# Kernel tuning notes

Hardware: AMD Instinct MI355X
Metric: run time of the kernel (lower is better)

Reference implementation:

```python
import jax, jax.numpy as jnp
import numpy as np

D_MODEL, D_FF, RANK = 1024, 4096, 256
B, S = 4, 4096


def setup_inputs() -> dict:
    key = jax.random.key(0)
    ks = jax.random.split(key, 7)
    return {
        "x":  jax.random.normal(ks[0], (B, S, D_MODEL), dtype=jnp.float32),
        "U1": jax.random.normal(ks[1], (D_MODEL, RANK), dtype=jnp.float32) * 0.02,
        "V1": jax.random.normal(ks[2], (RANK, D_FF), dtype=jnp.float32) * 0.02,
        "b1": jnp.zeros((D_FF,), dtype=jnp.float32),
        "U2": jax.random.normal(ks[3], (D_FF, RANK), dtype=jnp.float32) * 0.02,
        "V2": jax.random.normal(ks[4], (RANK, D_MODEL), dtype=jnp.float32) * 0.02,
        "b2": jnp.zeros((D_MODEL,), dtype=jnp.float32),
    }


def reference(x, U1, V1, b1, U2, V2, b2):
    # P = x @ U1  -> low-rank projection [B, S, rank]
    P = jnp.einsum("bsd,dr->bsr", x, U1)
    # H = gelu(P @ V1 + b1)  -> [B, S, d_ff] (the intermediate the flash kernel tiles over)
    H = jax.nn.gelu(jnp.einsum("bsr,rf->bsf", P, V1) + b1)
    # Q = H @ U2 -> [B, S, rank]; out = Q @ V2 + b2 -> [B, S, d_model]
    Q = jnp.einsum("bsf,fr->bsr", H, U2)
    return jnp.einsum("bsr,rd->bsd", Q, V2) + b2
```

## Files before the change

### kernel.cpp

```cpp
#include <hip/hip_runtime.h>
#include <hip/hip_bf16.h>


typedef __attribute__((ext_vector_type(8))) short bfrag8;
typedef __attribute__((ext_vector_type(4))) float fx4;
typedef __attribute__((ext_vector_type(4))) unsigned short usx4;

#define D_MODEL 1024
#define D_FF    4096
#define RANK    256
#define NROWS   16384
#define PSTR    264
#define XSTR    136

__device__ __forceinline__ unsigned short f2b(float f) {
  union { float f; unsigned u; } v; v.f = f;
  unsigned r = v.u + 0x7FFFu + ((v.u >> 16) & 1u);
  return (unsigned short)(r >> 16);
}

__device__ __forceinline__ float gelu_tanh(float x) {
  float x2 = x * x;
  float inner = __builtin_fmaf(0.044715f * x2, x, x);
  float e = __expf(1.5957691216057308f * inner);
  float t = __builtin_fmaf(-2.0f, __builtin_amdgcn_rcpf(1.0f + e), 1.0f);
  float hx = 0.5f * x;
  return __builtin_fmaf(hx, t, hx);
}

__device__ __forceinline__ void gl_lds16(const unsigned short* g, unsigned short* l) {
  __builtin_amdgcn_global_load_lds(
      (const __attribute__((address_space(1))) unsigned int*)g,
      (__attribute__((address_space(3))) unsigned int*)l, 16, 0, 0);
}

__global__ void tconv(const float* __restrict__ in, unsigned short* __restrict__ out,
                      int R, int C) {
  __shared__ float t[32][33];
  int c0 = blockIdx.x * 32, r0 = blockIdx.y * 32;
  int tx = threadIdx.x & 31, ty = threadIdx.x >> 5;
#pragma unroll
  for (int i = 0; i < 32; i += 8)
    t[ty + i][tx] = in[(size_t)(r0 + ty + i) * C + c0 + tx];
  __syncthreads();
#pragma unroll
  for (int i = 0; i < 32; i += 8)
    out[(size_t)(c0 + ty + i) * R + r0 + tx] = f2b(t[tx][ty + i]);
}

__global__ void v1pack(const float* __restrict__ in, unsigned short* __restrict__ out) {
  __shared__ float t[32][33];
  int f0 = blockIdx.x * 32, k0 = blockIdx.y * 32;
  int tx = threadIdx.x & 31, ty = threadIdx.x >> 5;
#pragma unroll
  for (int i = 0; i < 32; i += 8)
    t[ty + i][tx] = in[(size_t)(k0 + ty + i) * D_FF + f0 + tx];
  __syncthreads();
#pragma unroll
  for (int i = 0; i < 32; i += 8) {
    int f = ty + i;
    out[(size_t)(f0 + f) * RANK + ((k0 + tx) ^ ((f & 7) << 3))] = f2b(t[tx][f]);
  }
}

__global__ void u2pack(const float* __restrict__ in, unsigned short* __restrict__ out) {
  __shared__ float t[32][33];
  int f0 = blockIdx.x * 32, r0 = blockIdx.y * 32;
  int cg = blockIdx.x;
  int tx = threadIdx.x & 31, ty = threadIdx.x >> 5;
#pragma unroll
  for (int i = 0; i < 32; i += 8)
    t[ty + i][tx] = in[(size_t)(f0 + ty + i) * RANK + r0 + tx];
  __syncthreads();
#pragma unroll
  for (int i = 0; i < 32; i += 8) {
    int r2l = ty + i;
    int s = tx ^ (((r2l >> 1) & 3) << 3);
    int fl = (((s & 7) >= 4) ? 16 : 0) + 4 * (s >> 3) + (s & 3);
    out[(size_t)cg * 8192 + (size_t)(r0 + r2l) * 32 + tx] = f2b(t[fl][r2l]);
  }
}

__global__ __launch_bounds__(256, 4) void pgemm(
    const float* __restrict__ x, const unsigned short* __restrict__ u1t,
    unsigned short* __restrict__ P)
{
  __shared__ unsigned short xs[32 * XSTR];
  const int tid = threadIdx.x;
  const int w = tid >> 6, lane = tid & 63, lo = lane & 15, hi = lane >> 4;
  const size_t gr0 = (size_t)blockIdx.x * 32;

  fx4 acc[2][4];
#pragma unroll
  for (int mt = 0; mt < 2; ++mt)
#pragma unroll
    for (int nt = 0; nt < 4; ++nt) acc[mt][nt] = fx4{0.f, 0.f, 0.f, 0.f};

  for (int d0 = 0; d0 < D_MODEL; d0 += 128) {
    __syncthreads();
#pragma unroll
    for (int it = 0; it < 4; ++it) {
      int idx = it * 256 + tid;
      int r = idx >> 5, c = (idx & 31) << 2;
      fx4 v = *(const fx4*)(x + (gr0 + r) * D_MODEL + d0 + c);
      usx4 bv; bv[0] = f2b(v[0]); bv[1] = f2b(v[1]); bv[2] = f2b(v[2]); bv[3] = f2b(v[3]);
      *(usx4*)(xs + r * XSTR + c) = bv;
    }
    __syncthreads();
#pragma unroll
    for (int ks = 0; ks < 128; ks += 32) {
      bfrag8 a[2], b[4];
#pragma unroll
      for (int mt = 0; mt < 2; ++mt)
        a[mt] = *(const bfrag8*)(xs + (16 * mt + lo) * XSTR + ks + hi * 8);
#pragma unroll
      for (int nt = 0; nt < 4; ++nt)
        b[nt] = *(const bfrag8*)(u1t + (size_t)(w * 64 + nt * 16 + lo) * D_MODEL + d0 + ks + hi * 8);
#pragma unroll
      for (int mt = 0; mt < 2; ++mt)
#pragma unroll
        for (int nt = 0; nt < 4; ++nt)
          acc[mt][nt] = __builtin_amdgcn_mfma_f32_16x16x32_bf16(a[mt], b[nt], acc[mt][nt], 0, 0, 0);
    }
  }
#pragma unroll
  for (int mt = 0; mt < 2; ++mt)
#pragma unroll
    for (int nt = 0; nt < 4; ++nt)
#pragma unroll
      for (int r = 0; r < 4; ++r)
        P[(gr0 + 16 * mt + 4 * hi + r) * RANK + w * 64 + nt * 16 + lo] = f2b(acc[mt][nt][r]);
}

__global__ __launch_bounds__(256, 2) void hqgemm(
    const unsigned short* __restrict__ P,
    const unsigned short* __restrict__ v1c,
    const float* __restrict__ b1,
    const unsigned short* __restrict__ u2c,
    float* __restrict__ qpart,
    int F)
{
  __shared__ unsigned short v1s[2][32 * 256];
  __shared__ unsigned short u2s[2][256 * 32];

  const int tid = threadIdx.x;
  const int w = tid >> 6, lane = tid & 63, lo = lane & 15, hi = lane >> 4;

  int bid = blockIdx.x, j = 0, rb = bid;
  if (F == 4)      { j = bid & 3; rb = bid >> 2; }
  else if (F == 2) { j = bid & 1; rb = bid >> 1; }
  const int fbase = j * (D_FF / F);
  const int nchunk = (D_FF / F) / 32;
  const int rowstart = rb * 128 + w * 32;

  bfrag8 pf[2][8];
#pragma unroll
  for (int rg = 0; rg < 2; ++rg)
#pragma unroll
    for (int ks = 0; ks < 8; ++ks)
      pf[rg][ks] = *(const bfrag8*)(P + (size_t)(rowstart + 16 * rg + lo) * RANK + ks * 32 + hi * 8);

  fx4 qacc[2][16];
#pragma unroll
  for (int rg = 0; rg < 2; ++rg)
#pragma unroll
    for (int nt = 0; nt < 16; ++nt) qacc[rg][nt] = fx4{0.f, 0.f, 0.f, 0.f};

  const int vswz = (lo & 7) << 3;
  const int qoff = (hi * 8) ^ (((lo >> 1) & 3) << 3);
  const int vbase = lo * 256;

  {
    const unsigned short* vsrc = v1c + (size_t)fbase * 256;
    const unsigned short* usrc = u2c + (size_t)(fbase >> 5) * 8192;
#pragma unroll
    for (int p = 0; p < 4; ++p) {
      int off = tid * 8 + p * 2048;
      gl_lds16(vsrc + off, &v1s[0][off]);
      gl_lds16(usrc + off, &u2s[0][off]);
    }
  }
  __syncthreads();

  int cur = 0;
  for (int c = 0; c < nchunk; ++c) {
    if (c + 1 < nchunk) {
      const unsigned short* vsrc = v1c + (size_t)(fbase + (c + 1) * 32) * 256;
      const unsigned short* usrc = u2c + (size_t)((fbase >> 5) + c + 1) * 8192;
#pragma unroll
      for (int p = 0; p < 4; ++p) {
        int off = tid * 8 + p * 2048;
        gl_lds16(vsrc + off, &v1s[cur ^ 1][off]);
        gl_lds16(usrc + off, &u2s[cur ^ 1][off]);
      }
    }
    const unsigned short* vb = v1s[cur];
    const unsigned short* ub = u2s[cur];

    fx4 hacc[2][2];
#pragma unroll
    for (int t = 0; t < 2; ++t)
#pragma unroll
      for (int rg = 0; rg < 2; ++rg) hacc[t][rg] = fx4{0.f, 0.f, 0.f, 0.f};
#pragma unroll
    for (int ks = 0; ks < 8; ++ks) {
      int ko = (ks * 32 + hi * 8) ^ vswz;
      bfrag8 vE = *(const bfrag8*)(vb + vbase + ko);
      bfrag8 vO = *(const bfrag8*)(vb + vbase + 4096 + ko);
      hacc[0][0] = __builtin_amdgcn_mfma_f32_16x16x32_bf16(vE, pf[0][ks], hacc[0][0], 0, 0, 0);
      hacc[0][1] = __builtin_amdgcn_mfma_f32_16x16x32_bf16(vE, pf[1][ks], hacc[0][1], 0, 0, 0);
      hacc[1][0] = __builtin_amdgcn_mfma_f32_16x16x32_bf16(vO, pf[0][ks], hacc[1][0], 0, 0, 0);
      hacc[1][1] = __builtin_amdgcn_mfma_f32_16x16x32_bf16(vO, pf[1][ks], hacc[1][1], 0, 0, 0);
    }

    const int f0g = fbase + c * 32;
    fx4 bE = *(const fx4*)(b1 + f0g + 4 * hi);
    fx4 bO = *(const fx4*)(b1 + f0g + 16 + 4 * hi);
    bfrag8 bq0, bq1;
#pragma unroll
    for (int r = 0; r < 4; ++r) {
      bq0[r]     = (short)f2b(gelu_tanh(hacc[0][0][r] + bE[r]));
      bq0[r + 4] = (short)f2b(gelu_tanh(hacc[1][0][r] + bO[r]));
      bq1[r]     = (short)f2b(gelu_tanh(hacc[0][1][r] + bE[r]));
      bq1[r + 4] = (short)f2b(gelu_tanh(hacc[1][1][r] + bO[r]));
    }

#pragma unroll
    for (int nt = 0; nt < 16; ++nt) {
      bfrag8 qa = *(const bfrag8*)(ub + (16 * nt + lo) * 32 + qoff);
      qacc[0][nt] = __builtin_amdgcn_mfma_f32_16x16x32_bf16(qa, bq0, qacc[0][nt], 0, 0, 0);
      qacc[1][nt] = __builtin_amdgcn_mfma_f32_16x16x32_bf16(qa, bq1, qacc[1][nt], 0, 0, 0);
    }

    __syncthreads();
    cur ^= 1;
  }

  float* qp = qpart + (size_t)j * NROWS * RANK;
#pragma unroll
  for (int rg = 0; rg < 2; ++rg) {
    size_t row = (size_t)(rowstart + 16 * rg + lo);
#pragma unroll
    for (int nt = 0; nt < 16; ++nt)
      *(fx4*)(qp + row * RANK + 16 * nt + 4 * hi) = qacc[rg][nt];
  }
}

__global__ __launch_bounds__(512, 4) void ogemm(
    const float* __restrict__ qpart, int F,
    const unsigned short* __restrict__ v2t,
    const float* __restrict__ b2,
    float* __restrict__ out)
{
  __shared__ unsigned short Qs[64 * PSTR];
  const int tid = threadIdx.x;
  const int w = tid >> 6, lane = tid & 63, lo = lane & 15, hi = lane >> 4;
  const int wm = w >> 2, wn = w & 3;
  const size_t gr0 = (size_t)blockIdx.x * 64;
  const int n0 = blockIdx.y * 256;

#pragma unroll
  for (int it = 0; it < 8; ++it) {
    int idx = it * 512 + tid;
    int r = idx >> 6, c = (idx & 63) << 2;
    fx4 s = *(const fx4*)(qpart + (gr0 + r) * RANK + c);
    for (int jj = 1; jj < F; ++jj) {
      fx4 s1 = *(const fx4*)(qpart + (size_t)jj * NROWS * RANK + (gr0 + r) * RANK + c);
      s[0] += s1[0]; s[1] += s1[1]; s[2] += s1[2]; s[3] += s1[3];
    }
    usx4 bv; bv[0] = f2b(s[0]); bv[1] = f2b(s[1]); bv[2] = f2b(s[2]); bv[3] = f2b(s[3]);
    *(usx4*)(Qs + r * PSTR + c) = bv;
  }
  __syncthreads();

  fx4 acc[2][4];
#pragma unroll
  for (int mt = 0; mt < 2; ++mt)
#pragma unroll
    for (int nt = 0; nt < 4; ++nt) acc[mt][nt] = fx4{0.f, 0.f, 0.f, 0.f};

#pragma unroll
  for (int ks = 0; ks < RANK; ks += 32) {
    bfrag8 a[2], b[4];
#pragma unroll
    for (int mt = 0; mt < 2; ++mt)
      a[mt] = *(const bfrag8*)(Qs + (wm * 32 + 16 * mt + lo) * PSTR + ks + hi * 8);
#pragma unroll
    for (int nt = 0; nt < 4; ++nt)
      b[nt] = *(const bfrag8*)(v2t + (size_t)(n0 + wn * 64 + nt * 16 + lo) * RANK + ks + hi * 8);
#pragma unroll
    for (int mt = 0; mt < 2; ++mt)
#pragma unroll
      for (int nt = 0; nt < 4; ++nt)
        acc[mt][nt] = __builtin_amdgcn_mfma_f32_16x16x32_bf16(a[mt], b[nt], acc[mt][nt], 0, 0, 0);
  }

#pragma unroll
  for (int nt = 0; nt < 4; ++nt) {
    int col = n0 + wn * 64 + nt * 16 + lo;
    float bias = b2[col];
#pragma unroll
    for (int mt = 0; mt < 2; ++mt)
#pragma unroll
      for (int r = 0; r < 4; ++r)
        out[(gr0 + wm * 32 + 16 * mt + 4 * hi + r) * D_MODEL + col] = acc[mt][nt][r] + bias;
  }
}

extern "C" void kernel_launch(void* const* d_in, const int* in_sizes, int n_in,
                              void* d_out, int out_size, void* d_ws, size_t ws_size,
                              hipStream_t stream) {
  const float* x  = (const float*)d_in[0];
  const float* U1 = (const float*)d_in[1];
  const float* V1 = (const float*)d_in[2];
  const float* b1 = (const float*)d_in[3];
  const float* U2 = (const float*)d_in[4];
  const float* V2 = (const float*)d_in[5];
  const float* b2 = (const float*)d_in[6];
  float* out = (float*)d_out;

  unsigned short* ws16 = (unsigned short*)d_ws;
  unsigned short* u1t = ws16;
  unsigned short* v1c = u1t + (size_t)RANK * D_MODEL;
  unsigned short* u2c = v1c + (size_t)D_FF * RANK;
  unsigned short* v2t = u2c + (size_t)RANK * D_FF;
  unsigned short* Pbf = v2t + (size_t)D_MODEL * RANK;
  float* qpart = (float*)(Pbf + (size_t)NROWS * RANK);

  size_t fixed_bytes = 2ull * ((size_t)RANK * D_MODEL + (size_t)D_FF * RANK +
                               (size_t)RANK * D_FF + (size_t)D_MODEL * RANK +
                               (size_t)NROWS * RANK);
  size_t qbytes = (size_t)NROWS * RANK * 4;
  int F = 1;
  if      (ws_size >= fixed_bytes + 4 * qbytes) F = 4;
  else if (ws_size >= fixed_bytes + 2 * qbytes) F = 2;

  tconv<<<dim3(RANK / 32, D_MODEL / 32), 256, 0, stream>>>(U1, u1t, D_MODEL, RANK);
  v1pack<<<dim3(D_FF / 32, RANK / 32), 256, 0, stream>>>(V1, v1c);
  u2pack<<<dim3(D_FF / 32, RANK / 32), 256, 0, stream>>>(U2, u2c);
  tconv<<<dim3(D_MODEL / 32, RANK / 32), 256, 0, stream>>>(V2, v2t, RANK, D_MODEL);

  pgemm<<<NROWS / 32, 256, 0, stream>>>(x, u1t, Pbf);
  hqgemm<<<(NROWS / 128) * F, 256, 0, stream>>>(Pbf, v1c, b1, u2c, qpart, F);
  ogemm<<<dim3(NROWS / 64, D_MODEL / 256), 512, 0, stream>>>(qpart, F, v2t, b2, out);
}
```

Measured before the change: 202.5 us.

## Deepen hqgemm prefetch pipeline, store bf16 partials, and split F up to eight

Rewrites the hqgemm loop to keep two chunks in flight, using explicit vmcnt waits and raw barriers in place of __syncthreads, and adds s_setprio around the MFMA blocks. The bias is staged in LDS and GELU now uses exp2. Partial Q sums are stored as bf16 instead of fp32, which halves partial-sum traffic and lets F rise to 8 for more blocks in flight. The trade-off is extra rounding error in the partial sums and a fallback to F=4 that assumes enough workspace without checking.

Result: slower. 216.9 us (+7.1%).

```diff
diff --git a/kernel.cpp b/kernel.cpp
--- a/kernel.cpp
+++ b/kernel.cpp
@@ -18,11 +18,14 @@
   unsigned r = v.u + 0x7FFFu + ((v.u >> 16) & 1u);
   return (unsigned short)(r >> 16);
 }
+__device__ __forceinline__ float b2f(unsigned short u) {
+  union { unsigned u; float f; } v; v.u = ((unsigned)u) << 16; return v.f;
+}
 
 __device__ __forceinline__ float gelu_tanh(float x) {
   float x2 = x * x;
   float inner = __builtin_fmaf(0.044715f * x2, x, x);
-  float e = __expf(1.5957691216057308f * inner);
+  float e = __builtin_amdgcn_exp2f(2.302118885f * inner);
   float t = __builtin_fmaf(-2.0f, __builtin_amdgcn_rcpf(1.0f + e), 1.0f);
   float hx = 0.5f * x;
   return __builtin_fmaf(hx, t, hx);
@@ -137,20 +140,22 @@
     const unsigned short* __restrict__ v1c,
     const float* __restrict__ b1,
     const unsigned short* __restrict__ u2c,
-    float* __restrict__ qpart,
+    unsigned short* __restrict__ qpart,
     int F)
 {
   __shared__ unsigned short v1s[2][32 * 256];
   __shared__ unsigned short u2s[2][256 * 32];
+  __shared__ float b1s[1024];
 
   const int tid = threadIdx.x;
   const int w = tid >> 6, lane = tid & 63, lo = lane & 15, hi = lane >> 4;
 
-  int bid = blockIdx.x, j = 0, rb = bid;
-  if (F == 4)      { j = bid & 3; rb = bid >> 2; }
-  else if (F == 2) { j = bid & 1; rb = bid >> 1; }
-  const int fbase = j * (D_FF / F);
-  const int nchunk = (D_FF / F) / 32;
+  const int bid = blockIdx.x;
+  const int j = bid % F;
+  const int rb = bid / F;
+  const int fspan = D_FF / F;
+  const int fbase = j * fspan;
+  const int nchunk = fspan / 32;
   const int rowstart = rb * 128 + w * 32;
 
   bfrag8 pf[2][8];
@@ -159,6 +164,8 @@
 #pragma unroll
     for (int ks = 0; ks < 8; ++ks)
       pf[rg][ks] = *(const bfrag8*)(P + (size_t)(rowstart + 16 * rg + lo) * RANK + ks * 32 + hi * 8);
+  for (int i = tid; i < fspan; i += 256) b1s[i] = b1[fbase + i];
+  __syncthreads();
 
   fx4 qacc[2][16];
 #pragma unroll
@@ -170,30 +177,26 @@
   const int qoff = (hi * 8) ^ (((lo >> 1) & 3) << 3);
   const int vbase = lo * 256;
 
-  {
-    const unsigned short* vsrc = v1c + (size_t)fbase * 256;
-    const unsigned short* usrc = u2c + (size_t)(fbase >> 5) * 8192;
-#pragma unroll
-    for (int p = 0; p < 4; ++p) {
-      int off = tid * 8 + p * 2048;
-      gl_lds16(vsrc + off, &v1s[0][off]);
-      gl_lds16(usrc + off, &u2s[0][off]);
-    }
-  }
-  __syncthreads();
+#define HQ_STAGE(C, B) do {                                                    \
+    const unsigned short* vsrc_ = v1c + (size_t)(fbase + (C) * 32) * 256;      \
+    const unsigned short* usrc_ = u2c + (size_t)((fbase >> 5) + (C)) * 8192;   \
+    _Pragma("unroll")                                                          \
+    for (int p = 0; p < 4; ++p) {                                              \
+      int off_ = tid * 8 + p * 2048;                                           \
+      gl_lds16(vsrc_ + off_, &v1s[B][off_]);                                   \
+      gl_lds16(usrc_ + off_, &u2s[B][off_]);                                   \
+    } } while (0)
+
+  HQ_STAGE(0, 0);
+  if (nchunk > 1) HQ_STAGE(1, 1);
 
   int cur = 0;
   for (int c = 0; c < nchunk; ++c) {
-    if (c + 1 < nchunk) {
-      const unsigned short* vsrc = v1c + (size_t)(fbase + (c + 1) * 32) * 256;
-      const unsigned short* usrc = u2c + (size_t)((fbase >> 5) + c + 1) * 8192;
-#pragma unroll
-      for (int p = 0; p < 4; ++p) {
-        int off = tid * 8 + p * 2048;
-        gl_lds16(vsrc + off, &v1s[cur ^ 1][off]);
-        gl_lds16(usrc + off, &u2s[cur ^ 1][off]);
-      }
-    }
+    if (c + 1 < nchunk) asm volatile("s_waitcnt vmcnt(8)" ::: "memory");
+    else                asm volatile("s_waitcnt vmcnt(0)" ::: "memory");
+    asm volatile("s_barrier" ::: "memory");
+    __builtin_amdgcn_sched_barrier(0);
+
     const unsigned short* vb = v1s[cur];
     const unsigned short* ub = u2s[cur];
 
@@ -202,6 +205,7 @@
     for (int t = 0; t < 2; ++t)
 #pragma unroll
       for (int rg = 0; rg < 2; ++rg) hacc[t][rg] = fx4{0.f, 0.f, 0.f, 0.f};
+    __builtin_amdgcn_s_setprio(1);
 #pragma unroll
     for (int ks = 0; ks < 8; ++ks) {
       int ko = (ks * 32 + hi * 8) ^ vswz;
@@ -212,10 +216,10 @@
       hacc[1][0] = __builtin_amdgcn_mfma_f32_16x16x32_bf16(vO, pf[0][ks], hacc[1][0], 0, 0, 0);
       hacc[1][1] = __builtin_amdgcn_mfma_f32_16x16x32_bf16(vO, pf[1][ks], hacc[1][1], 0, 0, 0);
     }
-
-    const int f0g = fbase + c * 32;
-    fx4 bE = *(const fx4*)(b1 + f0g + 4 * hi);
-    fx4 bO = *(const fx4*)(b1 + f0g + 16 + 4 * hi);
+    __builtin_amdgcn_s_setprio(0);
+
+    fx4 bE = *(const fx4*)(&b1s[c * 32 + 4 * hi]);
+    fx4 bO = *(const fx4*)(&b1s[c * 32 + 16 + 4 * hi]);
     bfrag8 bq0, bq1;
 #pragma unroll
     for (int r = 0; r < 4; ++r) {
@@ -225,29 +229,38 @@
       bq1[r + 4] = (short)f2b(gelu_tanh(hacc[1][1][r] + bO[r]));
     }
 
+    __builtin_amdgcn_s_setprio(1);
 #pragma unroll
     for (int nt = 0; nt < 16; ++nt) {
       bfrag8 qa = *(const bfrag8*)(ub + (16 * nt + lo) * 32 + qoff);
       qacc[0][nt] = __builtin_amdgcn_mfma_f32_16x16x32_bf16(qa, bq0, qacc[0][nt], 0, 0, 0);
       qacc[1][nt] = __builtin_amdgcn_mfma_f32_16x16x32_bf16(qa, bq1, qacc[1][nt], 0, 0, 0);
     }
-
-    __syncthreads();
+    __builtin_amdgcn_s_setprio(0);
+
+    __builtin_amdgcn_sched_barrier(0);
+    asm volatile("s_barrier" ::: "memory");
+    if (c + 2 < nchunk) HQ_STAGE(c + 2, cur);
     cur ^= 1;
   }
-
-  float* qp = qpart + (size_t)j * NROWS * RANK;
+#undef HQ_STAGE
+
+  unsigned short* qp = qpart + (size_t)j * NROWS * RANK;
 #pragma unroll
   for (int rg = 0; rg < 2; ++rg) {
     size_t row = (size_t)(rowstart + 16 * rg + lo);
 #pragma unroll
-    for (int nt = 0; nt < 16; ++nt)
-      *(fx4*)(qp + row * RANK + 16 * nt + 4 * hi) = qacc[rg][nt];
+    for (int nt = 0; nt < 16; ++nt) {
+      usx4 qv;
+      qv[0] = f2b(qacc[rg][nt][0]); qv[1] = f2b(qacc[rg][nt][1]);
+      qv[2] = f2b(qacc[rg][nt][2]); qv[3] = f2b(qacc[rg][nt][3]);
+      *(usx4*)(qp + row * RANK + 16 * nt + 4 * hi) = qv;
+    }
   }
 }
 
 __global__ __launch_bounds__(512, 4) void ogemm(
-    const float* __restrict__ qpart, int F,
+    const unsigned short* __restrict__ qpart, int F,
     const unsigned short* __restrict__ v2t,
     const float* __restrict__ b2,
     float* __restrict__ out)
@@ -263,12 +276,12 @@
   for (int it = 0; it < 8; ++it) {
     int idx = it * 512 + tid;
     int r = idx >> 6, c = (idx & 63) << 2;
-    fx4 s = *(const fx4*)(qpart + (gr0 + r) * RANK + c);
-    for (int jj = 1; jj < F; ++jj) {
-      fx4 s1 = *(const fx4*)(qpart + (size_t)jj * NROWS * RANK + (gr0 + r) * RANK + c);
-      s[0] += s1[0]; s[1] += s1[1]; s[2] += s1[2]; s[3] += s1[3];
-    }
-    usx4 bv; bv[0] = f2b(s[0]); bv[1] = f2b(s[1]); bv[2] = f2b(s[2]); bv[3] = f2b(s[3]);
+    float s0 = 0.f, s1 = 0.f, s2 = 0.f, s3 = 0.f;
+    for (int jj = 0; jj < F; ++jj) {
+      usx4 q = *(const usx4*)(qpart + (size_t)jj * NROWS * RANK + (gr0 + r) * RANK + c);
+      s0 += b2f(q[0]); s1 += b2f(q[1]); s2 += b2f(q[2]); s3 += b2f(q[3]);
+    }
+    usx4 bv; bv[0] = f2b(s0); bv[1] = f2b(s1); bv[2] = f2b(s2); bv[3] = f2b(s3);
     *(usx4*)(Qs + r * PSTR + c) = bv;
   }
   __syncthreads();
@@ -325,15 +338,13 @@
   unsigned short* u2c = v1c + (size_t)D_FF * RANK;
   unsigned short* v2t = u2c + (size_t)RANK * D_FF;
   unsigned short* Pbf = v2t + (size_t)D_MODEL * RANK;
-  float* qpart = (float*)(Pbf + (size_t)NROWS * RANK);
+  unsigned short* qpart = Pbf + (size_t)NROWS * RANK;
 
   size_t fixed_bytes = 2ull * ((size_t)RANK * D_MODEL + (size_t)D_FF * RANK +
                                (size_t)RANK * D_FF + (size_t)D_MODEL * RANK +
                                (size_t)NROWS * RANK);
-  size_t qbytes = (size_t)NROWS * RANK * 4;
-  int F = 1;
-  if      (ws_size >= fixed_bytes + 4 * qbytes) F = 4;
-  else if (ws_size >= fixed_bytes + 2 * qbytes) F = 2;
+  size_t qb = (size_t)NROWS * RANK * 2;
+  int F = (ws_size >= fixed_bytes + 8 * qb) ? 8 : 4;
 
   tconv<<<dim3(RANK / 32, D_MODEL / 32), 256, 0, stream>>>(U1, u1t, D_MODEL, RANK);
   v1pack<<<dim3(D_FF / 32, RANK / 32), 256, 0, stream>>>(V1, v1c);
```
